# Kernel optimization log

Hardware: AMD Instinct MI355X
Metric: run time of the kernel (lower is better)

Reference implementation:

```python
import jax, jax.numpy as jnp
import numpy as np

MAX_LEN = 1024 * 16
D_MODEL = 512
N_HEADS = 8
D_HEAD = D_MODEL // N_HEADS
D_FF = 2048
SEQ = 2048
BATCH = 2
EPS = 1e-5


def setup_inputs() -> dict:
    key = jax.random.key(0)
    ks = jax.random.split(key, 12)
    s = 0.02
    return {
        "src": jax.random.normal(ks[0], (SEQ, BATCH, D_MODEL), jnp.float32),
        "Wq": jax.random.normal(ks[1], (D_MODEL, D_MODEL), jnp.float32) * s,
        "bq": jnp.zeros((D_MODEL,), jnp.float32),
        "Wk": jax.random.normal(ks[2], (D_MODEL, D_MODEL), jnp.float32) * s,
        "bk": jnp.zeros((D_MODEL,), jnp.float32),
        "Wv": jax.random.normal(ks[3], (D_MODEL, D_MODEL), jnp.float32) * s,
        "bv": jnp.zeros((D_MODEL,), jnp.float32),
        "Er": jax.random.normal(ks[4], (MAX_LEN, D_HEAD), jnp.float32) * s,
        "W1": jax.random.normal(ks[5], (D_MODEL, D_FF), jnp.float32) * s,
        "b1": jnp.zeros((D_FF,), jnp.float32),
        "W2": jax.random.normal(ks[6], (D_FF, D_MODEL), jnp.float32) * s,
        "b2": jnp.zeros((D_MODEL,), jnp.float32),
        "g1": jnp.ones((D_MODEL,), jnp.float32),
        "be1": jnp.zeros((D_MODEL,), jnp.float32),
        "g2": jnp.ones((D_MODEL,), jnp.float32),
        "be2": jnp.zeros((D_MODEL,), jnp.float32),
    }


def _layernorm(x, g, b):
    mu = jnp.mean(x, axis=-1, keepdims=True)
    var = jnp.mean(jnp.square(x - mu), axis=-1, keepdims=True)
    return (x - mu) * jax.lax.rsqrt(var + EPS) * g + b


def _skew(QEr):
    # QEr: [B, H, S, S] -> pad 1 on left of last dim, reshape, drop first row
    B, H, R, C = QEr.shape
    padded = jnp.pad(QEr, ((0, 0), (0, 0), (0, 0), (1, 0)))  # [B,H,R,C+1]
    reshaped = padded.reshape(B, H, C + 1, R)
    return reshaped[:, :, 1:, :]  # [B,H,R,C]


def _attention(x, Wq, bq, Wk, bk, Wv, bv, Er):
    B, S, _ = x.shape
    q = (x @ Wq + bq).reshape(B, S, N_HEADS, D_HEAD).transpose(0, 2, 1, 3)  # [B,H,S,dh]
    k = (x @ Wk + bk).reshape(B, S, N_HEADS, D_HEAD).transpose(0, 2, 1, 3)
    v = (x @ Wv + bv).reshape(B, S, N_HEADS, D_HEAD).transpose(0, 2, 1, 3)
    Er_t = Er[MAX_LEN - S:, :].T  # [dh, S]
    QEr = jnp.einsum("bhsd,dt->bhst", q, Er_t)  # [B,H,S,S]
    Srel = _skew(QEr)
    QK = jnp.einsum("bhsd,bhtd->bhst", q, k)
    attn = jax.nn.softmax((QK + Srel) / jnp.sqrt(jnp.float32(D_HEAD)), axis=-1)
    out = jnp.einsum("bhst,bhtd->bhsd", attn, v)
    return out.transpose(0, 2, 1, 3).reshape(B, S, D_MODEL)


def reference(src, Wq, bq, Wk, bk, Wv, bv, Er, W1, b1, W2, b2, g1, be1, g2, be2):
    # batch_first=False: [S,B,D] -> [B,S,D]
    x = jnp.transpose(src, (1, 0, 2))
    attn_out = _attention(x, Wq, bq, Wk, bk, Wv, bv, Er)
    # NOTE: original code does self.self_attn(...)[0], indexing batch element 0
    # of the returned tensor; it broadcasts over the batch dim. Replicated here.
    sa = attn_out[0]  # [S, D]
    x = _layernorm(x + sa, g1, be1)
    ff = jax.nn.relu(x @ W1 + b1) @ W2 + b2
    x = _layernorm(x + ff, g2, be2)
    return jnp.transpose(x, (1, 0, 2))  # back to [S,B,D]
```

## Files before the change

kernel.cpp:

```cpp
#include <hip/hip_runtime.h>

typedef __bf16 bf16;
typedef __attribute__((ext_vector_type(8))) __bf16 bf16x8;
typedef __attribute__((ext_vector_type(4))) __bf16 bf16x4;
typedef __attribute__((ext_vector_type(4))) float f32x4;

#define S 2048
#define DMODEL 512
#define NH 8
#define DH 64
#define DFF 2048
#define MAXLEN 16384
#define LN_EPS 1e-5f
#define NSP 8
#define CW (S / NSP)
#define BC 64
#define CST 0.18033688f

__device__ __forceinline__ void gload16(const bf16* g, bf16* l) {
  __builtin_amdgcn_global_load_lds(
      (const __attribute__((address_space(1))) void*)g,
      (__attribute__((address_space(3))) void*)l, 16, 0, 0);
}

template <int SWAP>
__global__ __launch_bounds__(256) void gemm_k(
    const bf16* __restrict__ A, long sAz, int lda,
    const bf16* __restrict__ B, long sBz, int ldb,
    void* __restrict__ C, long sCz, int ldc,
    const float* __restrict__ bias, long sBiasZ, int flags,
    int M, int N, int K, bf16* __restrict__ Ct)
{
  __shared__ bf16 lsA[128 * 32];
  __shared__ bf16 lsB[128 * 32];
  const int z = blockIdx.z;
  A += (long)z * sAz;
  B += (long)z * sBz;
  const int m0 = blockIdx.y * 128, n0 = blockIdx.x * 128;
  const int tid = threadIdx.x;
  const int lane = tid & 63, w = tid >> 6;
  const int wr = (w >> 1) * 64, wc = (w & 1) * 64;
  const int r15 = lane & 15, kg = lane >> 4;
  const int srow = lane >> 2, scol = (lane & 3) * 8;

  const bf16* Ag0 = A + (long)(m0 + 32 * w + srow) * lda + scol;
  const bf16* Ag1 = Ag0 + 16 * lda;
  const bf16* Bg0 = B + (long)(n0 + 32 * w + srow) * ldb + scol;
  const bf16* Bg1 = Bg0 + 16 * ldb;
  bf16* La0 = &lsA[(32 * w + srow) * 32 + scol];
  bf16* La1 = La0 + 16 * 32;
  bf16* Lb0 = &lsB[(32 * w + srow) * 32 + scol];
  bf16* Lb1 = Lb0 + 16 * 32;

  f32x4 acc[4][4] = {};
  for (int k0 = 0; k0 < K; k0 += 32) {
    gload16(Ag0 + k0, La0);
    gload16(Ag1 + k0, La1);
    gload16(Bg0 + k0, Lb0);
    gload16(Bg1 + k0, Lb1);
    __syncthreads();
    bf16x8 af[4], bfr[4];
#pragma unroll
    for (int mi = 0; mi < 4; ++mi) af[mi] = *(const bf16x8*)&lsA[(wr + mi * 16 + r15) * 32 + kg * 8];
#pragma unroll
    for (int ni = 0; ni < 4; ++ni) bfr[ni] = *(const bf16x8*)&lsB[(wc + ni * 16 + r15) * 32 + kg * 8];
    __builtin_amdgcn_s_setprio(1);
#pragma unroll
    for (int mi = 0; mi < 4; ++mi)
#pragma unroll
      for (int ni = 0; ni < 4; ++ni) {
        if (SWAP)
          acc[mi][ni] = __builtin_amdgcn_mfma_f32_16x16x32_bf16(bfr[ni], af[mi], acc[mi][ni], 0, 0, 0);
        else
          acc[mi][ni] = __builtin_amdgcn_mfma_f32_16x16x32_bf16(af[mi], bfr[ni], acc[mi][ni], 0, 0, 0);
      }
    __builtin_amdgcn_s_setprio(0);
    __syncthreads();
  }
  const float* bz = bias ? bias + (long)z * sBiasZ : nullptr;
  const float scl = ((flags & 4) && z == 0) ? CST : 1.f;

  if (SWAP) {
#pragma unroll
    for (int mi = 0; mi < 4; ++mi) {
      int row = m0 + wr + mi * 16 + r15;
#pragma unroll
      for (int ni = 0; ni < 4; ++ni) {
        int col0 = n0 + wc + ni * 16 + 4 * kg;
        float v[4];
#pragma unroll
        for (int r = 0; r < 4; ++r) {
          float bv = bz ? bz[col0 + r] : 0.f;
          v[r] = (acc[mi][ni][r] + bv) * scl;
          if (flags & 1) v[r] = fmaxf(v[r], 0.f);
        }
        long off = (long)z * sCz + (long)row * ldc + col0;
        if (flags & 2) {
          bf16x4 o = { (bf16)v[0], (bf16)v[1], (bf16)v[2], (bf16)v[3] };
          *(bf16x4*)&((bf16*)C)[off] = o;
        } else {
          f32x4 o = { v[0], v[1], v[2], v[3] };
          *(f32x4*)&((float*)C)[off] = o;
        }
      }
    }
  } else {
#pragma unroll
    for (int mi = 0; mi < 4; ++mi)
#pragma unroll
      for (int ni = 0; ni < 4; ++ni) {
        int col = n0 + wc + ni * 16 + r15;
        float bv = bz ? bz[col] : 0.f;
        float v[4];
#pragma unroll
        for (int r = 0; r < 4; ++r) {
          v[r] = (acc[mi][ni][r] + bv) * scl;
          if (flags & 1) v[r] = fmaxf(v[r], 0.f);
        }
        int rowb = m0 + wr + mi * 16 + kg * 4;
        if ((flags & 16) && z == 2) {
          bf16x4 o = { (bf16)v[0], (bf16)v[1], (bf16)v[2], (bf16)v[3] };
          *(bf16x4*)&Ct[(long)col * M + rowb] = o;
        } else {
#pragma unroll
          for (int r = 0; r < 4; ++r) {
            int row = rowb + r;
            if ((flags & 8) && row == 0 && col < N - 1) continue;
            if (flags & 2) ((bf16*)C)[(long)z * sCz + (long)row * ldc + col] = (bf16)v[r];
            else           ((float*)C)[(long)z * sCz + (long)row * ldc + col] = v[r];
          }
        }
      }
  }
}

__global__ __launch_bounds__(256) void prep_k(
    const float* __restrict__ src, const float* __restrict__ Er,
    const float* __restrict__ Wq, const float* __restrict__ Wk, const float* __restrict__ Wv,
    const float* __restrict__ W1, const float* __restrict__ W2,
    const float* __restrict__ bq, const float* __restrict__ bk, const float* __restrict__ bv,
    bf16* __restrict__ x0b, bf16* __restrict__ erS, bf16* __restrict__ srel,
    float* __restrict__ bqkv,
    bf16* __restrict__ wqkvT, bf16* __restrict__ w1T, bf16* __restrict__ w2T)
{
  __shared__ float t[32][33];
  const int bid = blockIdx.x, tid = threadIdx.x;
  if (bid < 4096) {
    long i = (long)bid * 256 + tid;
    int s2 = (int)(i >> 9), d = (int)(i & 511);
    x0b[i] = (bf16)src[(long)s2 * (2 * DMODEL) + d];
    return;
  }
  int b1_ = bid - 4096;
  if (b1_ < 512) {
    long i = (long)b1_ * 256 + tid;
    erS[i] = (bf16)Er[(long)(MAXLEN - S) * DH + i];
    return;
  }
  b1_ -= 512;
  if (b1_ < 64) {
    int i = b1_ * 256 + tid;
    if (i < NH * (S - 1)) {
      int h = i / (S - 1), rg = i - h * (S - 1);
      srel[(long)h * S * S + (long)rg * (S + 1) + 1] = (bf16)0.f;
    }
    return;
  }
  b1_ -= 64;
  if (b1_ < 6) {
    int ti = b1_ * 256 + tid;
    bqkv[ti] = ti < 512 ? bq[ti] : (ti < 1024 ? bk[ti - 512] : bv[ti - 1024]);
    return;
  }
  b1_ -= 6;
  const float* in;
  bf16* out;
  int R, Cn, bx, by;
  if (b1_ < 768) {
    int z = b1_ >> 8, rem = b1_ & 255;
    in = z == 0 ? Wq : (z == 1 ? Wk : Wv);
    out = wqkvT + (long)z * DMODEL * DMODEL;
    R = DMODEL; Cn = DMODEL; bx = rem & 15; by = rem >> 4;
  } else if (b1_ < 768 + 1024) {
    int rem = b1_ - 768;
    in = W1; out = w1T; R = DMODEL; Cn = DFF; bx = rem & 63; by = rem >> 6;
  } else {
    int rem = b1_ - 1792;
    in = W2; out = w2T; R = DFF; Cn = DMODEL; bx = rem & 15; by = rem >> 4;
  }
  int c0 = bx * 32, r0 = by * 32, tx = tid & 31, ty = tid >> 5;
#pragma unroll
  for (int i = 0; i < 32; i += 8) t[ty + i][tx] = in[(long)(r0 + ty + i) * Cn + c0 + tx];
  __syncthreads();
#pragma unroll
  for (int i = 0; i < 32; i += 8) out[(long)(c0 + ty + i) * R + r0 + tx] = (bf16)t[tx][ty + i];
}

__global__ __launch_bounds__(256, 5) void attn_k(
    const bf16* __restrict__ qg, const bf16* __restrict__ kgl, const bf16* __restrict__ vtg,
    const bf16* __restrict__ srel,
    bf16* __restrict__ pO, float* __restrict__ pM, float* __restrict__ pL)
{
  __shared__ bf16 Kl[64 * 72];
  __shared__ bf16 Vl[64 * 72];
  __shared__ bf16 SP[64 * 72];
  const int bx = blockIdx.x, h = blockIdx.y;
  const int rb = bx >> 3, sp = bx & 7;
  const int r0 = rb * 64;
  const int cb = sp * CW;
  const int tid = threadIdx.x, lane = tid & 63, w = tid >> 6;
  const int r15 = lane & 15, g = lane >> 4;
  const long hb = (long)h * S * S;

  bf16x8 qf0, qf1;
  {
    const bf16* qrow = qg + (long)(r0 + w * 16 + r15) * DMODEL + h * DH;
    qf0 = *(const bf16x8*)&qrow[g * 8];
    qf1 = *(const bf16x8*)&qrow[32 + g * 8];
  }
  f32x4 Oacc[4] = {};
  float m2 = -1e30f, l2 = 0.f;

  const int myrow = w * 16 + r15;
  const int rg = r0 + myrow;

  const int kRow = tid >> 3, kCh = (tid & 7) * 8;
  bf16x8 kf0, kf1, vf0, vf1, sf0, sf1;

  auto LOADR = [&](int c0) {
    kf0 = *(const bf16x8*)&kgl[(long)(c0 + kRow) * DMODEL + h * DH + kCh];
    kf1 = *(const bf16x8*)&kgl[(long)(c0 + kRow + 32) * DMODEL + h * DH + kCh];
    vf0 = *(const bf16x8*)&vtg[(long)(h * DH + kRow) * S + c0 + kCh];
    vf1 = *(const bf16x8*)&vtg[(long)(h * DH + kRow + 32) * S + c0 + kCh];
    sf0 = *(const bf16x8*)&srel[hb + (long)(r0 + kRow) * S + c0 + kCh];
    sf1 = *(const bf16x8*)&srel[hb + (long)(r0 + kRow + 32) * S + c0 + kCh];
  };
  auto STORE = [&]() {
    *(bf16x8*)&Kl[kRow * 72 + kCh] = kf0;
    *(bf16x8*)&Kl[(kRow + 32) * 72 + kCh] = kf1;
    *(bf16x8*)&Vl[kRow * 72 + kCh] = vf0;
    *(bf16x8*)&Vl[(kRow + 32) * 72 + kCh] = vf1;
    *(bf16x8*)&SP[kRow * 72 + kCh] = sf0;
    *(bf16x8*)&SP[(kRow + 32) * 72 + kCh] = sf1;
  };

  LOADR(cb);
#pragma unroll
  for (int t = 0; t < CW / BC; ++t) {
    __syncthreads();
    STORE();
    if (t + 1 < CW / BC) LOADR(cb + (t + 1) * BC);
    __syncthreads();

    f32x4 sc[4];
    __builtin_amdgcn_s_setprio(1);
#pragma unroll
    for (int ni = 0; ni < 4; ++ni) {
      bf16x8 k0f = *(const bf16x8*)&Kl[(ni * 16 + r15) * 72 + g * 8];
      bf16x8 k1f = *(const bf16x8*)&Kl[(ni * 16 + r15) * 72 + 32 + g * 8];
      f32x4 a = {};
      a = __builtin_amdgcn_mfma_f32_16x16x32_bf16(k0f, qf0, a, 0, 0, 0);
      a = __builtin_amdgcn_mfma_f32_16x16x32_bf16(k1f, qf1, a, 0, 0, 0);
      sc[ni] = a;
    }
    __builtin_amdgcn_s_setprio(0);

    const bf16* Sw = &SP[myrow * 72];
#pragma unroll
    for (int ni = 0; ni < 4; ++ni) {
      bf16x4 sv = *(const bf16x4*)&Sw[ni * 16 + 4 * g];
#pragma unroll
      for (int r = 0; r < 4; ++r) sc[ni][r] += (float)sv[r];
    }

    float tmax = sc[0][0];
#pragma unroll
    for (int ni = 0; ni < 4; ++ni)
#pragma unroll
      for (int r = 0; r < 4; ++r) tmax = fmaxf(tmax, sc[ni][r]);
    tmax = fmaxf(tmax, __shfl_xor(tmax, 16));
    tmax = fmaxf(tmax, __shfl_xor(tmax, 32));

    float mn = fmaxf(m2, tmax);
    float al = exp2f(m2 - mn);
    m2 = mn;
    float tsum = 0.f;
#pragma unroll
    for (int ni = 0; ni < 4; ++ni)
#pragma unroll
      for (int r = 0; r < 4; ++r) {
        float p = exp2f(sc[ni][r] - m2);
        sc[ni][r] = p;
        tsum += p;
      }
    tsum += __shfl_xor(tsum, 16);
    tsum += __shfl_xor(tsum, 32);
    l2 = l2 * al + tsum;

#pragma unroll
    for (int no = 0; no < 4; ++no)
#pragma unroll
      for (int r = 0; r < 4; ++r) Oacc[no][r] *= al;

    bf16* Pw = &SP[myrow * 72];
#pragma unroll
    for (int ni = 0; ni < 4; ++ni) {
      bf16x4 pv = { (bf16)sc[ni][0], (bf16)sc[ni][1], (bf16)sc[ni][2], (bf16)sc[ni][3] };
      *(bf16x4*)&Pw[ni * 16 + 4 * g] = pv;
    }

    __builtin_amdgcn_s_setprio(1);
#pragma unroll
    for (int kc = 0; kc < 2; ++kc) {
      bf16x8 pf = *(const bf16x8*)&SP[(w * 16 + r15) * 72 + kc * 32 + g * 8];
#pragma unroll
      for (int no = 0; no < 4; ++no) {
        bf16x8 av = *(const bf16x8*)&Vl[(no * 16 + r15) * 72 + kc * 32 + g * 8];
        Oacc[no] = __builtin_amdgcn_mfma_f32_16x16x32_bf16(av, pf, Oacc[no], 0, 0, 0);
      }
    }
    __builtin_amdgcn_s_setprio(0);
  }

  const long ob = ((long)sp * NH + h) * S * DH;
  const long qrow_g = r0 + w * 16 + r15;
#pragma unroll
  for (int no = 0; no < 4; ++no) {
    bf16x4 ov = { (bf16)Oacc[no][0], (bf16)Oacc[no][1], (bf16)Oacc[no][2], (bf16)Oacc[no][3] };
    *(bf16x4*)&pO[ob + qrow_g * DH + no * 16 + 4 * g] = ov;
  }
  if (g == 0) {
    const long sb = ((long)sp * NH + h) * S;
    pM[sb + rg] = m2;
    pL[sb + rg] = l2;
  }
}

__device__ __forceinline__ float blk_sum(float v, float* red) {
  for (int o = 32; o; o >>= 1) v += __shfl_xor(v, o);
  int tid = threadIdx.x;
  if ((tid & 63) == 0) red[tid >> 6] = v;
  __syncthreads();
  v = red[0] + red[1] + red[2] + red[3];
  __syncthreads();
  return v;
}

__global__ __launch_bounds__(256) void lnm1_k(
    const float* __restrict__ src, const bf16* __restrict__ pO,
    const float* __restrict__ pM, const float* __restrict__ pL,
    const float* __restrict__ g, const float* __restrict__ be, bf16* __restrict__ y)
{
  __shared__ float red[4];
  const int s2 = blockIdx.x, tid = threadIdx.x;
  float sa[2];
#pragma unroll
  for (int half = 0; half < 2; ++half) {
    int col = tid + half * 256;
    int h = col >> 6, d = col & 63;
    long i0 = (long)h * S + s2;
    float mm = -1e30f, ms[NSP];
#pragma unroll
    for (int s = 0; s < NSP; ++s) { ms[s] = pM[(long)s * NH * S + i0]; mm = fmaxf(mm, ms[s]); }
    float num = 0.f, den = 0.f;
#pragma unroll
    for (int s = 0; s < NSP; ++s) {
      float e = exp2f(ms[s] - mm);
      den += pL[(long)s * NH * S + i0] * e;
      num += (float)pO[(long)s * NH * S * DH + i0 * DH + d] * e;
    }
    sa[half] = num / den;
  }
#pragma unroll
  for (int b = 0; b < 2; ++b) {
    const float* xs = src + (long)s2 * (2 * DMODEL) + b * DMODEL;
    float a0 = xs[tid] + sa[0];
    float a1 = xs[tid + 256] + sa[1];
    float sum = blk_sum(a0 + a1, red);
    float sq  = blk_sum(a0 * a0 + a1 * a1, red);
    float mu = sum * (1.f / DMODEL);
    float var = sq * (1.f / DMODEL) - mu * mu;
    float rs = rsqrtf(var + LN_EPS);
    long ro = ((long)b * S + s2) * DMODEL;
    y[ro + tid]       = (bf16)((a0 - mu) * rs * g[tid] + be[tid]);
    y[ro + tid + 256] = (bf16)((a1 - mu) * rs * g[tid + 256] + be[tid + 256]);
  }
}

__global__ __launch_bounds__(256) void ln2_k(
    const bf16* __restrict__ y, const bf16* __restrict__ pFF, long pStride,
    const float* __restrict__ b2,
    const float* __restrict__ g, const float* __restrict__ be, float* __restrict__ out)
{
  __shared__ float red[4];
  const int row = blockIdx.x;
  const int b = row >> 11, s2 = row & 2047;
  const int tid = threadIdx.x;
  long i0 = (long)row * DMODEL + tid;
  long i1 = i0 + 256;
  float f0 = (float)pFF[i0] + (float)pFF[i0 + pStride] + (float)pFF[i0 + 2 * pStride] +
             (float)pFF[i0 + 3 * pStride] + b2[tid];
  float f1 = (float)pFF[i1] + (float)pFF[i1 + pStride] + (float)pFF[i1 + 2 * pStride] +
             (float)pFF[i1 + 3 * pStride] + b2[tid + 256];
  float a0 = (float)y[i0] + f0;
  float a1 = (float)y[i1] + f1;
  float sum = blk_sum(a0 + a1, red);
  float sq  = blk_sum(a0 * a0 + a1 * a1, red);
  float mu = sum * (1.f / DMODEL);
  float var = sq * (1.f / DMODEL) - mu * mu;
  float rs = rsqrtf(var + LN_EPS);
  float* o = out + (long)s2 * (2 * DMODEL) + b * DMODEL;
  o[tid]       = (a0 - mu) * rs * g[tid] + be[tid];
  o[tid + 256] = (a1 - mu) * rs * g[tid + 256] + be[tid + 256];
}

extern "C" void kernel_launch(void* const* d_in, const int* in_sizes, int n_in,
                              void* d_out, int out_size, void* d_ws, size_t ws_size,
                              hipStream_t stream)
{
  const float* src = (const float*)d_in[0];
  const float* Wq  = (const float*)d_in[1];
  const float* bq  = (const float*)d_in[2];
  const float* Wk  = (const float*)d_in[3];
  const float* bk  = (const float*)d_in[4];
  const float* Wv  = (const float*)d_in[5];
  const float* bv  = (const float*)d_in[6];
  const float* Er  = (const float*)d_in[7];
  const float* W1  = (const float*)d_in[8];
  const float* b1  = (const float*)d_in[9];
  const float* W2  = (const float*)d_in[10];
  const float* b2  = (const float*)d_in[11];
  const float* g1  = (const float*)d_in[12];
  const float* be1 = (const float*)d_in[13];
  const float* g2  = (const float*)d_in[14];
  const float* be2 = (const float*)d_in[15];

  char* wp = (char*)d_ws;
  auto alloc = [&](size_t bytes) { char* p = wp; wp += (bytes + 255) & ~(size_t)255; return p; };

  bf16* x0b   = (bf16*)alloc((size_t)S * DMODEL * 2);
  bf16* wqkvT = (bf16*)alloc((size_t)3 * DMODEL * DMODEL * 2);
  float* bqkv = (float*)alloc((size_t)3 * DMODEL * 4);
  bf16* w1T   = (bf16*)alloc((size_t)DFF * DMODEL * 2);
  bf16* w2T   = (bf16*)alloc((size_t)DMODEL * DFF * 2);
  bf16* erS   = (bf16*)alloc((size_t)S * DH * 2);
  bf16* qkvb  = (bf16*)alloc((size_t)3 * S * DMODEL * 2);
  bf16* vt    = (bf16*)alloc((size_t)DMODEL * S * 2);
  bf16* srel  = (bf16*)alloc((size_t)NH * S * S * 2);
  bf16* pO    = (bf16*)alloc((size_t)NSP * NH * S * DH * 2);
  float* pM   = (float*)alloc((size_t)NSP * NH * S * 4);
  float* pL   = (float*)alloc((size_t)NSP * NH * S * 4);
  bf16* yb    = (bf16*)alloc((size_t)2 * S * DMODEL * 2);
  bf16* h1    = (bf16*)alloc((size_t)2 * S * DFF * 2);
  bf16* pFF   = (bf16*)alloc((size_t)4 * 2 * S * DMODEL * 2);

  const long MN2 = (long)2 * S * DMODEL;

  prep_k<<<7494, 256, 0, stream>>>(src, Er, Wq, Wk, Wv, W1, W2, bq, bk, bv,
                                   x0b, erS, srel, bqkv, wqkvT, w1T, w2T);

  gemm_k<0><<<dim3(4, 16, 3), 256, 0, stream>>>(
      x0b, 0, DMODEL, wqkvT, (long)DMODEL * DMODEL, DMODEL,
      qkvb, (long)S * DMODEL, DMODEL, bqkv, DMODEL, 2 | 4 | 16, S, DMODEL, DMODEL, vt);

  const bf16* qb = qkvb;
  const bf16* kb = qkvb + (long)S * DMODEL;

  gemm_k<0><<<dim3(16, 16, 8), 256, 0, stream>>>(
      qb, DH, DMODEL, erS, 0, DH, (void*)(srel - (S - 1)), (long)S * S, S + 1,
      nullptr, 0, 2 | 8, S, S, DH, nullptr);

  attn_k<<<dim3(32 * NSP, NH), 256, 0, stream>>>(qb, kb, vt, srel, pO, pM, pL);

  lnm1_k<<<S, 256, 0, stream>>>(src, pO, pM, pL, g1, be1, yb);

  gemm_k<1><<<dim3(DFF / 128, (2 * S) / 128, 1), 256, 0, stream>>>(
      yb, 0, DMODEL, w1T, 0, DMODEL, h1, 0, DFF, b1, 0, 3, 2 * S, DFF, DMODEL, nullptr);

  gemm_k<1><<<dim3(DMODEL / 128, (2 * S) / 128, 4), 256, 0, stream>>>(
      h1, 512, DFF, w2T, 512, DFF, pFF, MN2, DMODEL, nullptr, 0, 2, 2 * S, DMODEL, 512, nullptr);

  ln2_k<<<2 * S, 256, 0, stream>>>(yb, pFF, MN2, b2, g2, be2, (float*)d_out);
}
```

Measured before the change: 153.7 us.

## Fuse relative-position skew into attention kernel, dropping materialized Srel tensor

```diff
diff --git a/kernel.cpp b/kernel.cpp
--- a/kernel.cpp
+++ b/kernel.cpp
@@ -16,6 +16,7 @@
 #define CW (S / NSP)
 #define BC 64
 #define CST 0.18033688f
+#define EBIG_ROWS 4096
 
 __device__ __forceinline__ void gload16(const bf16* g, bf16* l) {
   __builtin_amdgcn_global_load_lds(
@@ -125,7 +126,6 @@
 #pragma unroll
           for (int r = 0; r < 4; ++r) {
             int row = rowb + r;
-            if ((flags & 8) && row == 0 && col < N - 1) continue;
             if (flags & 2) ((bf16*)C)[(long)z * sCz + (long)row * ldc + col] = (bf16)v[r];
             else           ((float*)C)[(long)z * sCz + (long)row * ldc + col] = v[r];
           }
@@ -139,7 +139,7 @@
     const float* __restrict__ Wq, const float* __restrict__ Wk, const float* __restrict__ Wv,
     const float* __restrict__ W1, const float* __restrict__ W2,
     const float* __restrict__ bq, const float* __restrict__ bk, const float* __restrict__ bv,
-    bf16* __restrict__ x0b, bf16* __restrict__ erS, bf16* __restrict__ srel,
+    bf16* __restrict__ x0b, bf16* __restrict__ ebig,
     float* __restrict__ bqkv,
     bf16* __restrict__ wqkvT, bf16* __restrict__ w1T, bf16* __restrict__ w2T)
 {
@@ -152,21 +152,14 @@
     return;
   }
   int b1_ = bid - 4096;
-  if (b1_ < 512) {
+  if (b1_ < 1024) {
     long i = (long)b1_ * 256 + tid;
-    erS[i] = (bf16)Er[(long)(MAXLEN - S) * DH + i];
+    int u = (int)(i >> 6), k = (int)(i & 63);
+    int v = u >= (S + 1) ? u - (S + 1) : u;
+    ebig[i] = (v < S) ? (bf16)Er[(long)(MAXLEN - S + v) * DH + k] : (bf16)0.f;
     return;
   }
-  b1_ -= 512;
-  if (b1_ < 64) {
-    int i = b1_ * 256 + tid;
-    if (i < NH * (S - 1)) {
-      int h = i / (S - 1), rg = i - h * (S - 1);
-      srel[(long)h * S * S + (long)rg * (S + 1) + 1] = (bf16)0.f;
-    }
-    return;
-  }
-  b1_ -= 64;
+  b1_ -= 1024;
   if (b1_ < 6) {
     int ti = b1_ * 256 + tid;
     bqkv[ti] = ti < 512 ? bq[ti] : (ti < 1024 ? bk[ti - 512] : bv[ti - 1024]);
@@ -196,27 +189,30 @@
   for (int i = 0; i < 32; i += 8) out[(long)(c0 + ty + i) * R + r0 + tx] = (bf16)t[tx][ty + i];
 }
 
-__global__ __launch_bounds__(256, 5) void attn_k(
+__global__ __launch_bounds__(256, 4) void attn_k(
     const bf16* __restrict__ qg, const bf16* __restrict__ kgl, const bf16* __restrict__ vtg,
-    const bf16* __restrict__ srel,
+    const bf16* __restrict__ ebig,
     bf16* __restrict__ pO, float* __restrict__ pM, float* __restrict__ pL)
 {
   __shared__ bf16 Kl[64 * 72];
   __shared__ bf16 Vl[64 * 72];
-  __shared__ bf16 SP[64 * 72];
+  __shared__ bf16 Hl[66 * 136];
   const int bx = blockIdx.x, h = blockIdx.y;
   const int rb = bx >> 3, sp = bx & 7;
   const int r0 = rb * 64;
   const int cb = sp * CW;
   const int tid = threadIdx.x, lane = tid & 63, w = tid >> 6;
   const int r15 = lane & 15, g = lane >> 4;
-  const long hb = (long)h * S * S;
-
-  bf16x8 qf0, qf1;
+
+  bf16x8 qf0, qf1, qe0, qe1;
   {
     const bf16* qrow = qg + (long)(r0 + w * 16 + r15) * DMODEL + h * DH;
     qf0 = *(const bf16x8*)&qrow[g * 8];
     qf1 = *(const bf16x8*)&qrow[32 + g * 8];
+    int q2 = r0 + 64 + r15; if (q2 > S - 1) q2 = S - 1;
+    const bf16* qrow2 = qg + (long)q2 * DMODEL + h * DH;
+    qe0 = *(const bf16x8*)&qrow2[g * 8];
+    qe1 = *(const bf16x8*)&qrow2[32 + g * 8];
   }
   f32x4 Oacc[4] = {};
   float m2 = -1e30f, l2 = 0.f;
@@ -225,28 +221,26 @@
   const int rg = r0 + myrow;
 
   const int kRow = tid >> 3, kCh = (tid & 7) * 8;
-  bf16x8 kf0, kf1, vf0, vf1, sf0, sf1;
+  bf16x8 kf0, kf1, vf0, vf1;
 
   auto LOADR = [&](int c0) {
     kf0 = *(const bf16x8*)&kgl[(long)(c0 + kRow) * DMODEL + h * DH + kCh];
     kf1 = *(const bf16x8*)&kgl[(long)(c0 + kRow + 32) * DMODEL + h * DH + kCh];
     vf0 = *(const bf16x8*)&vtg[(long)(h * DH + kRow) * S + c0 + kCh];
     vf1 = *(const bf16x8*)&vtg[(long)(h * DH + kRow + 32) * S + c0 + kCh];
-    sf0 = *(const bf16x8*)&srel[hb + (long)(r0 + kRow) * S + c0 + kCh];
-    sf1 = *(const bf16x8*)&srel[hb + (long)(r0 + kRow + 32) * S + c0 + kCh];
   };
   auto STORE = [&]() {
     *(bf16x8*)&Kl[kRow * 72 + kCh] = kf0;
     *(bf16x8*)&Kl[(kRow + 32) * 72 + kCh] = kf1;
     *(bf16x8*)&Vl[kRow * 72 + kCh] = vf0;
     *(bf16x8*)&Vl[(kRow + 32) * 72 + kCh] = vf1;
-    *(bf16x8*)&SP[kRow * 72 + kCh] = sf0;
-    *(bf16x8*)&SP[(kRow + 32) * 72 + kCh] = sf1;
   };
 
   LOADR(cb);
 #pragma unroll
   for (int t = 0; t < CW / BC; ++t) {
+    const int c0 = cb + t * BC;
+    const int ub = S - 64 + c0 - r0;
     __syncthreads();
     STORE();
     if (t + 1 < CW / BC) LOADR(cb + (t + 1) * BC);
@@ -263,15 +257,45 @@
       a = __builtin_amdgcn_mfma_f32_16x16x32_bf16(k1f, qf1, a, 0, 0, 0);
       sc[ni] = a;
     }
+
+    const bf16* eb = ebig + (long)ub * DH;
+#pragma unroll
+    for (int ni = 0; ni < 8; ++ni) {
+      bf16x8 e0 = *(const bf16x8*)&eb[(ni * 16 + r15) * DH + g * 8];
+      bf16x8 e1 = *(const bf16x8*)&eb[(ni * 16 + r15) * DH + 32 + g * 8];
+      f32x4 a = {};
+      a = __builtin_amdgcn_mfma_f32_16x16x32_bf16(e0, qf0, a, 0, 0, 0);
+      a = __builtin_amdgcn_mfma_f32_16x16x32_bf16(e1, qf1, a, 0, 0, 0);
+      bf16x4 hv = { (bf16)a[0], (bf16)a[1], (bf16)a[2], (bf16)a[3] };
+      *(bf16x4*)&Hl[myrow * 136 + ni * 16 + 4 * g] = hv;
+    }
+    if (w == 0) {
+#pragma unroll
+      for (int ni = 0; ni < 8; ++ni) {
+        bf16x8 e0 = *(const bf16x8*)&eb[(ni * 16 + r15) * DH + g * 8];
+        bf16x8 e1 = *(const bf16x8*)&eb[(ni * 16 + r15) * DH + 32 + g * 8];
+        f32x4 a = {};
+        a = __builtin_amdgcn_mfma_f32_16x16x32_bf16(e0, qe0, a, 0, 0, 0);
+        a = __builtin_amdgcn_mfma_f32_16x16x32_bf16(e1, qe1, a, 0, 0, 0);
+        if (r15 == 0) {
+          bf16x4 hv = { (bf16)a[0], (bf16)a[1], (bf16)a[2], (bf16)a[3] };
+          *(bf16x4*)&Hl[64 * 136 + ni * 16 + 4 * g] = hv;
+        }
+      }
+    }
     __builtin_amdgcn_s_setprio(0);
-
-    const bf16* Sw = &SP[myrow * 72];
-#pragma unroll
-    for (int ni = 0; ni < 4; ++ni) {
-      bf16x4 sv = *(const bf16x4*)&Sw[ni * 16 + 4 * g];
-#pragma unroll
-      for (int r = 0; r < 4; ++r) sc[ni][r] += (float)sv[r];
-    }
+    __syncthreads();
+
+    const int cthr = r0 - c0 + myrow + 1;
+    const int hbase = myrow * 136 + 63 - myrow;
+#pragma unroll
+    for (int ni = 0; ni < 4; ++ni)
+#pragma unroll
+      for (int r = 0; r < 4; ++r) {
+        int cl = ni * 16 + 4 * g + r;
+        int a = hbase + cl + ((cl >= cthr) ? 136 : 0);
+        sc[ni][r] += (float)Hl[a];
+      }
 
     float tmax = sc[0][0];
 #pragma unroll
@@ -302,7 +326,7 @@
 #pragma unroll
       for (int r = 0; r < 4; ++r) Oacc[no][r] *= al;
 
-    bf16* Pw = &SP[myrow * 72];
+    bf16* Pw = &Kl[myrow * 72];
 #pragma unroll
     for (int ni = 0; ni < 4; ++ni) {
       bf16x4 pv = { (bf16)sc[ni][0], (bf16)sc[ni][1], (bf16)sc[ni][2], (bf16)sc[ni][3] };
@@ -312,7 +336,7 @@
     __builtin_amdgcn_s_setprio(1);
 #pragma unroll
     for (int kc = 0; kc < 2; ++kc) {
-      bf16x8 pf = *(const bf16x8*)&SP[(w * 16 + r15) * 72 + kc * 32 + g * 8];
+      bf16x8 pf = *(const bf16x8*)&Kl[myrow * 72 + kc * 32 + g * 8];
 #pragma unroll
       for (int no = 0; no < 4; ++no) {
         bf16x8 av = *(const bf16x8*)&Vl[(no * 16 + r15) * 72 + kc * 32 + g * 8];
@@ -443,10 +467,9 @@
   float* bqkv = (float*)alloc((size_t)3 * DMODEL * 4);
   bf16* w1T   = (bf16*)alloc((size_t)DFF * DMODEL * 2);
   bf16* w2T   = (bf16*)alloc((size_t)DMODEL * DFF * 2);
-  bf16* erS   = (bf16*)alloc((size_t)S * DH * 2);
+  bf16* ebig  = (bf16*)alloc((size_t)EBIG_ROWS * DH * 2);
   bf16* qkvb  = (bf16*)alloc((size_t)3 * S * DMODEL * 2);
   bf16* vt    = (bf16*)alloc((size_t)DMODEL * S * 2);
-  bf16* srel  = (bf16*)alloc((size_t)NH * S * S * 2);
   bf16* pO    = (bf16*)alloc((size_t)NSP * NH * S * DH * 2);
   float* pM   = (float*)alloc((size_t)NSP * NH * S * 4);
   float* pL   = (float*)alloc((size_t)NSP * NH * S * 4);
@@ -456,8 +479,8 @@
 
   const long MN2 = (long)2 * S * DMODEL;
 
-  prep_k<<<7494, 256, 0, stream>>>(src, Er, Wq, Wk, Wv, W1, W2, bq, bk, bv,
-                                   x0b, erS, srel, bqkv, wqkvT, w1T, w2T);
+  prep_k<<<7942, 256, 0, stream>>>(src, Er, Wq, Wk, Wv, W1, W2, bq, bk, bv,
+                                   x0b, ebig, bqkv, wqkvT, w1T, w2T);
 
   gemm_k<0><<<dim3(4, 16, 3), 256, 0, stream>>>(
       x0b, 0, DMODEL, wqkvT, (long)DMODEL * DMODEL, DMODEL,
@@ -466,11 +489,7 @@
   const bf16* qb = qkvb;
   const bf16* kb = qkvb + (long)S * DMODEL;
 
-  gemm_k<0><<<dim3(16, 16, 8), 256, 0, stream>>>(
-      qb, DH, DMODEL, erS, 0, DH, (void*)(srel - (S - 1)), (long)S * S, S + 1,
-      nullptr, 0, 2 | 8, S, S, DH, nullptr);
-
-  attn_k<<<dim3(32 * NSP, NH), 256, 0, stream>>>(qb, kb, vt, srel, pO, pM, pL);
+  attn_k<<<dim3(32 * NSP, NH), 256, 0, stream>>>(qb, kb, vt, ebig, pO, pM, pL);
 
   lnm1_k<<<S, 256, 0, stream>>>(src, pO, pM, pL, g1, be1, yb);
 
```

Result: slower. 190.0 us (+23.6%).
